# Performance work log

Hardware: AMD Instinct MI355X
Metric: run time of the kernel (lower is better)

The kernel has to match this reference:

```python
import jax, jax.numpy as jnp
import numpy as np

B = 131072   # batch
D = 16       # input_dim
L1 = 4       # num lattices in layer 1 (= ceil(D / DPL))
DPL = 4      # input_dim_per_lattice
E = 24       # output_size (ensemble columns)
K = 16       # calibrator keypoints per feature
NV = 2 ** DPL  # hypercube corners per lattice (lattice_keypoints=2 per dim)


def setup_inputs() -> dict:
    key = jax.random.key(0)
    k1, k2, k3, k4, k5 = jax.random.split(key, 5)
    x = jax.random.normal(k1, (B, D), jnp.float32)
    # piecewise-linear calibrators: sorted input keypoints, monotone outputs in [0,1]
    cal_kp = jnp.sort(jax.random.uniform(k2, (D, K), jnp.float32, -3.0, 3.0), axis=-1)
    raw = jax.random.uniform(k3, (D, K), jnp.float32, 0.1, 1.0)
    cv = jnp.cumsum(raw, axis=-1)
    cal_vals = (cv - cv[:, :1]) / (cv[:, -1:] - cv[:, :1])  # [D,K] in [0,1], increasing
    kernels1 = jax.random.uniform(k4, (E, L1, NV), jnp.float32)  # per-column layer-1 lattice vertices
    kernels2 = jax.random.uniform(k5, (E, 1, NV), jnp.float32)   # per-column layer-2 lattice vertices
    return {"x": x, "cal_kp": cal_kp, "cal_vals": cal_vals,
            "kernels1": kernels1, "kernels2": kernels2}


def _mlin_weights(xg):
    """Multilinear (HYPERCUBE) interpolation weights for unit lattices.
    xg: [..., L, d] with entries in [0,1]. Returns [..., L, 2^d] corner weights,
    corner index with dim 0 as most-significant bit."""
    d = xg.shape[-1]
    w = jnp.ones(xg.shape[:-1] + (1,), xg.dtype)
    for i in range(d):
        xi = xg[..., i]                              # [..., L]
        pair = jnp.stack([1.0 - xi, xi], axis=-1)    # [..., L, 2]
        w = (w[..., :, None] * pair[..., None, :]).reshape(*xg.shape[:-1], -1)
    return w


def reference(x, cal_kp, cal_vals, kernels1, kernels2):
    # 1) calibrate_and_stack: per-feature piecewise-linear calibration to [0,1]
    xc = jax.vmap(jnp.interp)(x.T, cal_kp, cal_vals).T           # [B, D]
    # 2) layer 1: split D dims into L1 lattices of DPL dims each (clip_inputs=True)
    xg1 = jnp.clip(xc.reshape(-1, L1, DPL), 0.0, 1.0)            # [B, L1, DPL]
    w1 = _mlin_weights(xg1)                                      # [B, L1, 2^DPL]
    h1 = jnp.einsum('blk,elk->ebl', w1, kernels1)                # [E, B, L1]
    # 3) layer 2: one lattice of DPL dims per ensemble column
    xg2 = jnp.clip(h1[:, :, None, :], 0.0, 1.0)                  # [E, B, 1, DPL]
    w2 = _mlin_weights(xg2)                                      # [E, B, 1, 2^DPL]
    out = jnp.einsum('eblk,elk->be', w2, kernels2)               # [B, E]
    return out
```

## Files before the change

### kernel.cpp

```cpp
#include <hip/hip_runtime.h>


typedef _Float16 f16x4 __attribute__((ext_vector_type(4)));
typedef float f32x4 __attribute__((ext_vector_type(4)));

namespace {
constexpr int kD = 16, kE = 24, kK = 16, kNV = 16;
constexpr int kThreads = 256;
constexpr int kRPB = 64;
constexpr int kK2S = 20;
}

__global__ __launch_bounds__(kThreads, 6) void lattice_fwd(
    const float* __restrict__ x,
    const float* __restrict__ cal_kp,
    const float* __restrict__ cal_vals,
    const float* __restrict__ k1,
    const float* __restrict__ k2,
    float* __restrict__ out)
{
    __shared__ float sKp[kD * 16];
    __shared__ f32x4 sEnt[kD * 16];
    __shared__ f16x4 sW[4 * 4 * 64];
    __shared__ f16x4 sK1[4 * 2 * 64];
    __shared__ float sK2[32 * kK2S];

    const int tid  = threadIdx.x;
    const int lane = tid & 63;
    const int wv   = __builtin_amdgcn_readfirstlane(tid >> 6);

    const size_t row = (size_t)blockIdx.x * kRPB + lane;
    f32x4 xin = *reinterpret_cast<const f32x4*>(x + row * kD + wv * 4);

    sKp[tid] = ((tid & 15) == 15) ? __builtin_inff() : cal_kp[tid];
    if (tid < kD * 15) {
        int d = tid / 15;
        int k = tid - d * 15;
        float kp0 = cal_kp[d * kK + k];
        float kp1 = cal_kp[d * kK + k + 1];
        float v0  = cal_vals[d * kK + k];
        float v1  = cal_vals[d * kK + k + 1];
        float dxv = kp1 - kp0;
        float slope = (dxv > 0.0f) ? (v1 - v0) / dxv : 0.0f;
        sEnt[d * 16 + k] = (f32x4){kp0, slope, v0, 0.0f};
    }
    #pragma unroll
    for (int s0 = 0; s0 < 2; ++s0) {
        int s  = tid + s0 * kThreads;
        int l  = s >> 7;
        int n  = (s >> 6) & 1;
        int ls = s & 63;
        int e  = n * 16 + (ls & 15);
        int g  = ls >> 4;
        f16x4 v = {(_Float16)0.f, (_Float16)0.f, (_Float16)0.f, (_Float16)0.f};
        if (e < kE) {
            const float* src = k1 + ((size_t)(e * 4 + l) * kNV + 4 * g);
            v[0] = (_Float16)src[0]; v[1] = (_Float16)src[1];
            v[2] = (_Float16)src[2]; v[3] = (_Float16)src[3];
        }
        sK1[s] = v;
    }
    {
        int e = tid >> 3, j = tid & 7;
        float a = 0.f, b = 0.f;
        if (e < kE) { a = k2[e * kNV + j]; b = k2[e * kNV + j + 8]; }
        sK2[e * kK2S + j]     = a;
        sK2[e * kK2S + j + 8] = b;
    }

    __syncthreads();

    float xc[4];
    #pragma unroll
    for (int i = 0; i < 4; ++i) {
        const int d = wv * 4 + i;
        const float xv = xin[i];
        const float* kpb = &sKp[d * 16];
        int j = 0;
        #pragma unroll
        for (int s = 8; s >= 1; s >>= 1) {
            float kps = kpb[j + s];
            j = (xv >= kps) ? j + s : j;
        }
        f32x4 ent = sEnt[d * 16 + j];
        float t = fmaf(ent[1], xv - ent[0], ent[2]);
        xc[i] = fminf(fmaxf(t, 0.0f), 1.0f);
    }

    float wf[16];
    {
        float a = xc[0], b = xc[1], c = xc[2], d = xc[3];
        float t2[2] = {1.0f - a, a};
        float t4[4];
        #pragma unroll
        for (int j = 0; j < 2; ++j) { t4[2*j] = t2[j]*(1.0f-b); t4[2*j+1] = t2[j]*b; }
        float t8[8];
        #pragma unroll
        for (int j = 0; j < 4; ++j) { t8[2*j] = t4[j]*(1.0f-c); t8[2*j+1] = t4[j]*c; }
        #pragma unroll
        for (int j = 0; j < 8; ++j) { wf[2*j] = t8[j]*(1.0f-d); wf[2*j+1] = t8[j]*d; }
    }

    {
        int m = lane >> 4, r15 = lane & 15;
        #pragma unroll
        for (int g = 0; g < 4; ++g) {
            f16x4 v;
            v[0] = (_Float16)wf[4*g+0]; v[1] = (_Float16)wf[4*g+1];
            v[2] = (_Float16)wf[4*g+2]; v[3] = (_Float16)wf[4*g+3];
            sW[(m * 4 + wv) * 64 + r15 + 16 * g] = v;
        }
    }

    __syncthreads();

    f16x4 af[4];
    #pragma unroll
    for (int l = 0; l < 4; ++l) af[l] = sW[(wv * 4 + l) * 64 + lane];

    const size_t outBase = (size_t)blockIdx.x * kRPB + wv * 16;

    #pragma unroll
    for (int n = 0; n < 2; ++n) {
        const int e = n * 16 + (lane & 15);
        const bool valid = (e < kE);

        f16x4 bf[4];
        #pragma unroll
        for (int l = 0; l < 4; ++l) bf[l] = sK1[(l * 2 + n) * 64 + lane];

        float kb[16];
        {
            const f32x4* kp2 = reinterpret_cast<const f32x4*>(&sK2[e * kK2S]);
            #pragma unroll
            for (int j = 0; j < 4; ++j) {
                f32x4 t = kp2[j];
                kb[4*j+0]=t[0]; kb[4*j+1]=t[1]; kb[4*j+2]=t[2]; kb[4*j+3]=t[3];
            }
        }
        float db[8];
        #pragma unroll
        for (int j = 0; j < 8; ++j) db[j] = kb[2*j+1] - kb[2*j];

        f32x4 acc[4];
        #pragma unroll
        for (int l = 0; l < 4; ++l)
            acc[l] = __builtin_amdgcn_mfma_f32_16x16x16f16(
                af[l], bf[l], (f32x4){0.f, 0.f, 0.f, 0.f}, 0, 0, 0);

        #pragma unroll
        for (int r = 0; r < 4; ++r) {
            float h0 = fminf(fmaxf(acc[0][r], 0.0f), 1.0f);
            float h1 = fminf(fmaxf(acc[1][r], 0.0f), 1.0f);
            float h2 = fminf(fmaxf(acc[2][r], 0.0f), 1.0f);
            float h3 = fminf(fmaxf(acc[3][r], 0.0f), 1.0f);
            float v8[8];
            #pragma unroll
            for (int j = 0; j < 8; ++j) v8[j] = fmaf(h3, db[j], kb[2*j]);
            float v4[4];
            #pragma unroll
            for (int j = 0; j < 4; ++j) v4[j] = fmaf(h2, v8[2*j+1]-v8[2*j], v8[2*j]);
            float v2[2];
            #pragma unroll
            for (int j = 0; j < 2; ++j) v2[j] = fmaf(h1, v4[2*j+1]-v4[2*j], v4[2*j]);
            float o = fmaf(h0, v2[1]-v2[0], v2[0]);
            if (valid) {
                size_t orow = outBase + ((lane >> 4) << 2) + r;
                out[orow * kE + e] = o;
            }
        }
    }
}

extern "C" void kernel_launch(void* const* d_in, const int* in_sizes, int n_in,
                              void* d_out, int out_size, void* d_ws, size_t ws_size,
                              hipStream_t stream) {
    const float* x        = (const float*)d_in[0];
    const float* cal_kp   = (const float*)d_in[1];
    const float* cal_vals = (const float*)d_in[2];
    const float* k1       = (const float*)d_in[3];
    const float* k2       = (const float*)d_in[4];
    float* out = (float*)d_out;

    hipLaunchKernelGGL(lattice_fwd, dim3(131072 / kRPB), dim3(kThreads), 0, stream,
                       x, cal_kp, cal_vals, k1, k2, out);
}
```

Baseline: 14.73 us.

## Remap rows so each wave owns its tile, drop barrier, pack layer-2 math

Each wave now loads the x rows for its own 16-row tile, with lanes split across the four lattices, instead of one feature group per wave. The weight exchange through shared memory then stays inside a wave, so the second __syncthreads is replaced by an lgkmcnt wait. Layer-2 kernel differences are precomputed during staging, and the layer-2 interpolation runs on float2 vectors, which may let the compiler emit packed FMA. Occupancy hint is lowered from 6 to 5. The x loads become less coalesced per lane group, and correctness now depends on the wave-local ordering of LDS accesses.

Result: faster. 14.23 us (-3.4%).

```diff
diff --git a/kernel.cpp b/kernel.cpp
--- a/kernel.cpp
+++ b/kernel.cpp
@@ -3,6 +3,7 @@
 
 typedef _Float16 f16x4 __attribute__((ext_vector_type(4)));
 typedef float f32x4 __attribute__((ext_vector_type(4)));
+typedef float f32x2 __attribute__((ext_vector_type(2)));
 
 namespace {
 constexpr int kD = 16, kE = 24, kK = 16, kNV = 16;
@@ -11,7 +12,26 @@
 constexpr int kK2S = 20;
 }
 
-__global__ __launch_bounds__(kThreads, 6) void lattice_fwd(
+static __device__ __forceinline__ f32x2 fma2(f32x2 a, f32x2 b, f32x2 c) {
+#if __has_builtin(__builtin_elementwise_fma)
+    return __builtin_elementwise_fma(a, b, c);
+#else
+    return (f32x2){fmaf(a[0], b[0], c[0]), fmaf(a[1], b[1], c[1])};
+#endif
+}
+static __device__ __forceinline__ f32x2 fma2s(f32x2 a, float b, float c) {
+    return fma2(a, (f32x2){b, b}, (f32x2){c, c});
+}
+static __device__ __forceinline__ f32x2 clamp01(f32x2 v) {
+#if __has_builtin(__builtin_elementwise_max) && __has_builtin(__builtin_elementwise_min)
+    return __builtin_elementwise_min(
+        __builtin_elementwise_max(v, (f32x2){0.f, 0.f}), (f32x2){1.f, 1.f});
+#else
+    return (f32x2){fminf(fmaxf(v[0], 0.f), 1.f), fminf(fmaxf(v[1], 0.f), 1.f)};
+#endif
+}
+
+__global__ __launch_bounds__(kThreads, 5) void lattice_fwd(
     const float* __restrict__ x,
     const float* __restrict__ cal_kp,
     const float* __restrict__ cal_vals,
@@ -28,9 +48,13 @@
     const int tid  = threadIdx.x;
     const int lane = tid & 63;
     const int wv   = __builtin_amdgcn_readfirstlane(tid >> 6);
-
-    const size_t row = (size_t)blockIdx.x * kRPB + lane;
-    f32x4 xin = *reinterpret_cast<const f32x4*>(x + row * kD + wv * 4);
+    const int q    = lane >> 4;
+    const int r15  = lane & 15;
+
+    const int rowBase = blockIdx.x * kRPB + wv * 16;
+
+    f32x4 xin = *reinterpret_cast<const f32x4*>(
+        x + (size_t)(rowBase + r15) * kD + 4 * q);
 
     sKp[tid] = ((tid & 15) == 15) ? __builtin_inff() : cal_kp[tid];
     if (tid < kD * 15) {
@@ -62,10 +86,10 @@
     }
     {
         int e = tid >> 3, j = tid & 7;
-        float a = 0.f, b = 0.f;
-        if (e < kE) { a = k2[e * kNV + j]; b = k2[e * kNV + j + 8]; }
-        sK2[e * kK2S + j]     = a;
-        sK2[e * kK2S + j + 8] = b;
+        float lo = 0.f, hi = 0.f;
+        if (e < kE) { lo = k2[e * kNV + 2 * j]; hi = k2[e * kNV + 2 * j + 1]; }
+        sK2[e * kK2S + j]     = lo;
+        sK2[e * kK2S + 8 + j] = hi - lo;
     }
 
     __syncthreads();
@@ -73,7 +97,7 @@
     float xc[4];
     #pragma unroll
     for (int i = 0; i < 4; ++i) {
-        const int d = wv * 4 + i;
+        const int d = 4 * q + i;
         const float xv = xin[i];
         const float* kpb = &sKp[d * 16];
         int j = 0;
@@ -101,46 +125,34 @@
         for (int j = 0; j < 8; ++j) { wf[2*j] = t8[j]*(1.0f-d); wf[2*j+1] = t8[j]*d; }
     }
 
-    {
-        int m = lane >> 4, r15 = lane & 15;
-        #pragma unroll
-        for (int g = 0; g < 4; ++g) {
-            f16x4 v;
-            v[0] = (_Float16)wf[4*g+0]; v[1] = (_Float16)wf[4*g+1];
-            v[2] = (_Float16)wf[4*g+2]; v[3] = (_Float16)wf[4*g+3];
-            sW[(m * 4 + wv) * 64 + r15 + 16 * g] = v;
-        }
-    }
-
-    __syncthreads();
+    #pragma unroll
+    for (int g = 0; g < 4; ++g) {
+        f16x4 v;
+        v[0] = (_Float16)wf[4*g+0]; v[1] = (_Float16)wf[4*g+1];
+        v[2] = (_Float16)wf[4*g+2]; v[3] = (_Float16)wf[4*g+3];
+        sW[(wv * 4 + q) * 64 + r15 + 16 * g] = v;
+    }
+    asm volatile("s_waitcnt lgkmcnt(0)" ::: "memory");
 
     f16x4 af[4];
     #pragma unroll
     for (int l = 0; l < 4; ++l) af[l] = sW[(wv * 4 + l) * 64 + lane];
 
-    const size_t outBase = (size_t)blockIdx.x * kRPB + wv * 16;
-
     #pragma unroll
     for (int n = 0; n < 2; ++n) {
-        const int e = n * 16 + (lane & 15);
-        const bool valid = (e < kE);
+        const int e = n * 16 + r15;
 
         f16x4 bf[4];
         #pragma unroll
         for (int l = 0; l < 4; ++l) bf[l] = sK1[(l * 2 + n) * 64 + lane];
 
-        float kb[16];
-        {
-            const f32x4* kp2 = reinterpret_cast<const f32x4*>(&sK2[e * kK2S]);
-            #pragma unroll
-            for (int j = 0; j < 4; ++j) {
-                f32x4 t = kp2[j];
-                kb[4*j+0]=t[0]; kb[4*j+1]=t[1]; kb[4*j+2]=t[2]; kb[4*j+3]=t[3];
-            }
-        }
-        float db[8];
-        #pragma unroll
-        for (int j = 0; j < 8; ++j) db[j] = kb[2*j+1] - kb[2*j];
+        const float* kr = &sK2[e * kK2S];
+        f32x4 ke0 = *reinterpret_cast<const f32x4*>(kr);
+        f32x4 ke1 = *reinterpret_cast<const f32x4*>(kr + 4);
+        f32x4 kd0 = *reinterpret_cast<const f32x4*>(kr + 8);
+        f32x4 kd1 = *reinterpret_cast<const f32x4*>(kr + 12);
+        float kbe[8] = {ke0[0],ke0[1],ke0[2],ke0[3], ke1[0],ke1[1],ke1[2],ke1[3]};
+        float db [8] = {kd0[0],kd0[1],kd0[2],kd0[3], kd1[0],kd1[1],kd1[2],kd1[3]};
 
         f32x4 acc[4];
         #pragma unroll
@@ -149,24 +161,25 @@
                 af[l], bf[l], (f32x4){0.f, 0.f, 0.f, 0.f}, 0, 0, 0);
 
         #pragma unroll
-        for (int r = 0; r < 4; ++r) {
-            float h0 = fminf(fmaxf(acc[0][r], 0.0f), 1.0f);
-            float h1 = fminf(fmaxf(acc[1][r], 0.0f), 1.0f);
-            float h2 = fminf(fmaxf(acc[2][r], 0.0f), 1.0f);
-            float h3 = fminf(fmaxf(acc[3][r], 0.0f), 1.0f);
-            float v8[8];
+        for (int p = 0; p < 2; ++p) {
+            f32x2 h0 = clamp01((f32x2){acc[0][2*p], acc[0][2*p+1]});
+            f32x2 h1 = clamp01((f32x2){acc[1][2*p], acc[1][2*p+1]});
+            f32x2 h2 = clamp01((f32x2){acc[2][2*p], acc[2][2*p+1]});
+            f32x2 h3 = clamp01((f32x2){acc[3][2*p], acc[3][2*p+1]});
+            f32x2 v8[8];
             #pragma unroll
-            for (int j = 0; j < 8; ++j) v8[j] = fmaf(h3, db[j], kb[2*j]);
-            float v4[4];
+            for (int j = 0; j < 8; ++j) v8[j] = fma2s(h3, db[j], kbe[j]);
+            f32x2 v4[4];
             #pragma unroll
-            for (int j = 0; j < 4; ++j) v4[j] = fmaf(h2, v8[2*j+1]-v8[2*j], v8[2*j]);
-            float v2[2];
+            for (int j = 0; j < 4; ++j) v4[j] = fma2(h2, v8[2*j+1]-v8[2*j], v8[2*j]);
+            f32x2 v2[2];
             #pragma unroll
-            for (int j = 0; j < 2; ++j) v2[j] = fmaf(h1, v4[2*j+1]-v4[2*j], v4[2*j]);
-            float o = fmaf(h0, v2[1]-v2[0], v2[0]);
-            if (valid) {
-                size_t orow = outBase + ((lane >> 4) << 2) + r;
-                out[orow * kE + e] = o;
+            for (int j = 0; j < 2; ++j) v2[j] = fma2(h1, v4[2*j+1]-v4[2*j], v4[2*j]);
+            f32x2 o = fma2(h0, v2[1]-v2[0], v2[0]);
+            if (e < kE) {
+                size_t r0 = (size_t)(rowBase + q * 4 + 2 * p);
+                out[r0 * kE + e]       = o[0];
+                out[(r0 + 1) * kE + e] = o[1];
             }
         }
     }
```
